# Kernel optimization log

Measured on AMD Instinct MI355X. Metric: run time of the kernel, lower is better.

The kernel has to match this reference:

```python
import jax, jax.numpy as jnp
import numpy as np

B, H_IMG, W_IMG = 8, 64, 64
C, HEADS, SR, MSG = 128, 4, 4, 4
N0 = H_IMG * W_IMG


def _linear(x, w, b):
    return x @ w.T + b


def _layernorm(x, g, b, eps=1e-5):
    mu = jnp.mean(x, -1, keepdims=True)
    var = jnp.mean(jnp.square(x - mu), -1, keepdims=True)
    return (x - mu) * jax.lax.rsqrt(var + eps) * g + b


def _conv2d(x, w, b, stride, pad, groups=1):
    y = jax.lax.conv_general_dilated(
        x, w, (stride, stride), [(pad, pad), (pad, pad)],
        dimension_numbers=("NCHW", "OIHW", "NCHW"), feature_group_count=groups)
    return y + b[None, :, None, None]


def setup_inputs():
    key = jax.random.key(0)
    ks = jax.random.split(key, 16)
    def nrm(k, shape, std=0.02):
        return jax.random.normal(k, shape, jnp.float32) * std
    z = lambda *s: jnp.zeros(s, jnp.float32)
    return {
        "x": jax.random.normal(ks[0], (B, N0, C), jnp.float32),
        "msg_tokens": jax.random.normal(ks[1], (B, MSG, C), jnp.float32),
        "Wq": nrm(ks[2], (C, C)), "bq": z(C),
        "sr1_w": nrm(ks[3], (C, C, 4, 4), float(np.sqrt(2.0 / (16 * C)))), "sr1_b": z(C),
        "ln1_g": jnp.ones((C,), jnp.float32), "ln1_b": z(C),
        "sr2_w": nrm(ks[4], (C, C, 2, 2), float(np.sqrt(2.0 / (4 * C)))), "sr2_b": z(C),
        "ln2_g": jnp.ones((C,), jnp.float32), "ln2_b": z(C),
        "kv1_w": nrm(ks[5], (C, C)), "kv1_b": z(C),
        "kv2_w": nrm(ks[6], (C, C)), "kv2_b": z(C),
        "lc1_w": nrm(ks[7], (C // 2, 1, 3, 3), float(np.sqrt(2.0 / 9.0))), "lc1_b": z(C // 2),
        "lc2_w": nrm(ks[8], (C // 2, 1, 3, 3), float(np.sqrt(2.0 / 9.0))), "lc2_b": z(C // 2),
        "proj_w": nrm(ks[9], (C, C)), "proj_b": z(C),
        "H": H_IMG, "W": W_IMG,
    }


def reference(x, msg_tokens, Wq, bq, sr1_w, sr1_b, ln1_g, ln1_b,
              sr2_w, sr2_b, ln2_g, ln2_b, kv1_w, kv1_b, kv2_w, kv2_b,
              lc1_w, lc1_b, lc2_w, lc2_b, proj_w, proj_b, H, W):
    Bsz, _, Cc = x.shape
    m = msg_tokens.shape[1]
    h = HEADS
    dh = Cc // h
    scale = dh ** -0.5
    x_q = jnp.concatenate([x, msg_tokens], axis=1)       # [B, N, C]
    N = x_q.shape[1]
    q = _linear(x_q, Wq, bq).reshape(Bsz, N, h, dh).transpose(0, 2, 1, 3)  # [B,h,N,dh]
    x_img = x.transpose(0, 2, 1).reshape(Bsz, Cc, H, W)

    def branch(sr_w, sr_b, ln_g, ln_b, kv_w, kv_b, lc_w, lc_b, q_half, stride):
        Hr, Wr = H // stride, W // stride
        L = Hr * Wr
        # spatial reduction conv -> tokens
        xr = _conv2d(x_img, sr_w, sr_b, stride, 0).reshape(Bsz, Cc, L).transpose(0, 2, 1)
        # message tokens pass through the SR conv via summed weights
        msg_r = jnp.einsum('bnc,oc->bno', msg_tokens, sr_w.sum((-1, -2))) + sr_b
        xk = jax.nn.gelu(_layernorm(jnp.concatenate([xr, msg_r], 1), ln_g, ln_b), approximate=False)
        kv = _linear(xk, kv_w, kv_b).reshape(Bsz, L + m, 2, h // 2, dh).transpose(2, 0, 3, 1, 4)
        k, v = kv[0], kv[1]                               # [B, h/2, L+m, dh]
        attn = jax.nn.softmax(jnp.einsum('bhnd,bhld->bhnl', q_half, k) * scale, axis=-1)
        # fused depthwise conv on the spatial part of V (message tokens bypass)
        v_flat = v.transpose(0, 2, 1, 3).reshape(Bsz, L + m, Cc // 2).transpose(0, 2, 1)  # [B,C/2,L+m]
        lc = _conv2d(v_flat[:, :, :L].reshape(Bsz, Cc // 2, Hr, Wr), lc_w, lc_b, 1, 1,
                     groups=Cc // 2).reshape(Bsz, Cc // 2, L)
        v_add = jnp.concatenate([lc, v_flat[:, :, L:]], axis=2)
        v = v + v_add.reshape(Bsz, h // 2, dh, L + m).transpose(0, 1, 3, 2)
        return jnp.einsum('bhnl,bhld->bhnd', attn, v).transpose(0, 2, 1, 3).reshape(Bsz, N, Cc // 2)

    x1 = branch(sr1_w, sr1_b, ln1_g, ln1_b, kv1_w, kv1_b, lc1_w, lc1_b, q[:, :h // 2], SR)
    x2 = branch(sr2_w, sr2_b, ln2_g, ln2_b, kv2_w, kv2_b, lc2_w, lc2_b, q[:, h // 2:], SR // 2)
    out = _linear(jnp.concatenate([x1, x2], -1), proj_w, proj_b)
    out = x_q + out                                       # identity = x_q, drop_path = Identity
    return out[:, :-m], out[:, -m:]
```

## Files before the change

kernel.cpp:

```cpp
#include <hip/hip_runtime.h>
#include <math.h>

#define BB 8
#define CC 128
#define N0 4096
#define MSGN 4
#define NTOT 4100
#define IMG 64
#define NPAD 4112
#define QTILES 257
#define LMP1 320
#define LMP2 1088

#define OFF_WFQ    0
#define OFF_WFKV1  8192
#define OFF_WFKV2  16384
#define OFF_WFPROJ 24576
#define OFF_WFSR1  32768
#define OFF_WFSR2  163840
#define OFF_QH     196608
#define OFF_XA     2301952
#define OFF_XK1    6565888
#define OFF_XK2    6701056
#define OFF_KV1O   7229440
#define OFF_KV2O   7495680
#define OFF_KH1    8548352
#define OFF_VT1    8630272
#define OFF_KH2    8712192
#define OFF_VT2    8990720

typedef _Float16 half8v __attribute__((ext_vector_type(8)));
typedef _Float16 half4v __attribute__((ext_vector_type(4)));
typedef float f32x4 __attribute__((ext_vector_type(4)));

__device__ __forceinline__ size_t af_idx(int m, int k, int Kc) {
    return ((size_t)((m >> 4) * Kc + (k >> 5)) * 64 + ((k >> 3) & 3) * 16 + (m & 15)) * 8 + (k & 7);
}

__global__ void prep_weights(const float* __restrict__ Wq, const float* __restrict__ kv1,
                             const float* __restrict__ kv2, const float* __restrict__ proj,
                             const float* __restrict__ sr1w, const float* __restrict__ sr2w,
                             float* __restrict__ ws, _Float16* __restrict__ Qh) {
    int u = blockIdx.x * blockDim.x + threadIdx.x;
    if (u >= 49152) {
        int idx = u - 49152;
        if (idx >= BB * 4 * (NPAD - NTOT) * 32) return;
        int d = idx & 31;
        int rest = idx >> 5;
        int n = NTOT + rest % (NPAD - NTOT);
        int rest2 = rest / (NPAD - NTOT);
        int hg = rest2 & 3;
        int b = rest2 >> 2;
        Qh[((size_t)(b * 4 + hg) * NPAD + n) * 32 + d] = (_Float16)0.f;
        return;
    }
    int seg, base;
    const float* w = nullptr;
    _Float16* dst;
    if (u < 2048)        { seg = 0; base = u;          w = Wq;   dst = (_Float16*)(ws + OFF_WFQ); }
    else if (u < 4096)   { seg = 0; base = u - 2048;   w = kv1;  dst = (_Float16*)(ws + OFF_WFKV1); }
    else if (u < 6144)   { seg = 0; base = u - 4096;   w = kv2;  dst = (_Float16*)(ws + OFF_WFKV2); }
    else if (u < 8192)   { seg = 0; base = u - 6144;   w = proj; dst = (_Float16*)(ws + OFF_WFPROJ); }
    else if (u < 40960)  { seg = 1; base = u - 8192;   w = sr1w; dst = (_Float16*)(ws + OFF_WFSR1); }
    else                 { seg = 2; base = u - 40960;  w = sr2w; dst = (_Float16*)(ws + OFF_WFSR2); }
    int lane = base & 63;
    int t = (base >> 6) & 7;
    int kc = base >> 9;
    int n = t * 16 + (lane & 15);
    int k0 = kc * 32 + (lane >> 4) * 8;
    half8v val;
    #pragma unroll
    for (int j = 0; j < 8; ++j) {
        int k = k0 + j;
        float v;
        if (seg == 0) v = w[n * 128 + k];
        else if (seg == 1) v = w[(n * 128 + (k & 127)) * 16 + (k >> 7)];
        else v = w[(n * 128 + (k & 127)) * 4 + (k >> 7)];
        val[j] = (_Float16)v;
    }
    *(half8v*)(dst + (size_t)base * 8) = val;
}

__global__ __launch_bounds__(256) void qproj_gemm(
    const float* __restrict__ x, const float* __restrict__ msg,
    const _Float16* __restrict__ Wf, const float* __restrict__ bias,
    _Float16* __restrict__ Qh) {
    int lane = threadIdx.x & 63, wave = threadIdx.x >> 6;
    int mt = blockIdx.x * 4 + wave;
    int m15 = lane & 15, quadk = lane >> 4;
    int m = mt * 16 + m15;
    bool valid = m < BB * NTOT;
    const float* rowp = x;
    if (valid) {
        int b = m / NTOT, n = m - b * NTOT;
        rowp = (n < N0) ? (x + ((size_t)b * N0 + n) * 128)
                        : (msg + ((size_t)b * MSGN + (n - N0)) * 128);
    }
    const half8v* Bp = (const half8v*)Wf + lane;
    f32x4 acc[8];
    #pragma unroll
    for (int t = 0; t < 8; ++t) acc[t] = (f32x4){0.f, 0.f, 0.f, 0.f};
    #pragma unroll
    for (int kc = 0; kc < 4; ++kc) {
        half8v a;
        if (valid) {
            const float4* p4 = (const float4*)(rowp + (kc * 4 + quadk) * 8);
            float4 f0 = p4[0], f1 = p4[1];
            a[0] = (_Float16)f0.x; a[1] = (_Float16)f0.y; a[2] = (_Float16)f0.z; a[3] = (_Float16)f0.w;
            a[4] = (_Float16)f1.x; a[5] = (_Float16)f1.y; a[6] = (_Float16)f1.z; a[7] = (_Float16)f1.w;
        } else {
            #pragma unroll
            for (int j = 0; j < 8; ++j) a[j] = (_Float16)0.f;
        }
        #pragma unroll
        for (int t = 0; t < 8; ++t)
            acc[t] = __builtin_amdgcn_mfma_f32_16x16x32_f16(a, Bp[(size_t)(kc * 8 + t) * 64], acc[t], 0, 0, 0);
    }
    int quad = lane >> 4, n15 = lane & 15;
    const float qscale = 0.17677669529663687f;
    #pragma unroll
    for (int r = 0; r < 4; ++r) {
        int mm = mt * 16 + quad * 4 + r;
        if (mm >= BB * NTOT) continue;
        int b = mm / NTOT, tok = mm - b * NTOT;
        #pragma unroll
        for (int t = 0; t < 8; ++t) {
            int n = t * 16 + n15;
            Qh[((size_t)(b * 4 + (n >> 5)) * NPAD + tok) * 32 + (n & 31)] =
                (_Float16)((acc[t][r] + bias[n]) * qscale);
        }
    }
}

template<int S, int WR, int LL, int LM, int KW>
__device__ __forceinline__ void sr_partial(
    int mtile, int kcbase, int lane, const float* __restrict__ x,
    const float* __restrict__ msg, const _Float16* __restrict__ Wf, f32x4 acc[8]) {
    int m15 = lane & 15, quadk = lane >> 4;
    int m = mtile * 16 + m15;
    bool valid = m < BB * LM;
    const float* base = x;
    bool isimg = false;
    if (valid) {
        int b = m / LM, tok = m - b * LM;
        if (tok < LL) {
            int hr = tok / WR, wr = tok - hr * WR;
            base = x + ((size_t)b * N0 + hr * S * IMG + wr * S) * 128;
            isimg = true;
        } else {
            base = msg + ((size_t)b * MSGN + (tok - LL)) * 128;
        }
    }
    const half8v* Bp = (const half8v*)Wf + lane;
    for (int kk = 0; kk < KW; ++kk) {
        int kc = kcbase + kk;
        int k0 = (kc * 4 + quadk) * 8;
        int c = k0 & 127, ij = k0 >> 7;
        half8v a;
        if (valid) {
            int off;
            if (isimg) {
                int ki = ij / S, kj = ij - ki * S;
                off = (ki * IMG + kj) * 128 + c;
            } else off = c;
            const float4* p4 = (const float4*)(base + off);
            float4 f0 = p4[0], f1 = p4[1];
            a[0] = (_Float16)f0.x; a[1] = (_Float16)f0.y; a[2] = (_Float16)f0.z; a[3] = (_Float16)f0.w;
            a[4] = (_Float16)f1.x; a[5] = (_Float16)f1.y; a[6] = (_Float16)f1.z; a[7] = (_Float16)f1.w;
        } else {
            #pragma unroll
            for (int j = 0; j < 8; ++j) a[j] = (_Float16)0.f;
        }
        #pragma unroll
        for (int t = 0; t < 8; ++t)
            acc[t] = __builtin_amdgcn_mfma_f32_16x16x32_f16(a, Bp[(size_t)(kc * 8 + t) * 64], acc[t], 0, 0, 0);
    }
}

__global__ __launch_bounds__(256) void sr_gemm(
    const float* __restrict__ x, const float* __restrict__ msg,
    const _Float16* __restrict__ Wf1, const _Float16* __restrict__ Wf2,
    const float* __restrict__ b1, const float* __restrict__ g1, const float* __restrict__ be1,
    const float* __restrict__ b2, const float* __restrict__ g2, const float* __restrict__ be2,
    _Float16* __restrict__ XK1, _Float16* __restrict__ XK2) {
    __shared__ float red[4][2048];
    int tid = threadIdx.x;
    int lane = tid & 63, wave = tid >> 6;
    int bid = blockIdx.x;
    f32x4 acc[8];
    #pragma unroll
    for (int t = 0; t < 8; ++t) acc[t] = (f32x4){0.f, 0.f, 0.f, 0.f};
    const float* bias;
    const float* lng;
    const float* lnb;
    _Float16* outp;
    int mtile, Mv;
    if (bid < 132) {
        mtile = bid; Mv = 2080;
        sr_partial<4, 16, 256, 260, 16>(mtile, wave * 16, lane, x, msg, Wf1, acc);
        bias = b1; lng = g1; lnb = be1; outp = XK1;
    } else {
        mtile = bid - 132; Mv = 8224;
        sr_partial<2, 32, 1024, 1028, 4>(mtile, wave * 4, lane, x, msg, Wf2, acc);
        bias = b2; lng = g2; lnb = be2; outp = XK2;
    }
    int quad = lane >> 4, n15 = lane & 15;
    #pragma unroll
    for (int t = 0; t < 8; ++t)
        #pragma unroll
        for (int r = 0; r < 4; ++r)
            red[wave][(quad * 4 + r) * 128 + t * 16 + n15] = acc[t][r];
    __syncthreads();
    for (int e = tid; e < 2048; e += 256)
        red[0][e] = red[0][e] + red[1][e] + red[2][e] + red[3][e];
    __syncthreads();
    int r16 = tid >> 4, l16 = tid & 15;
    int m = mtile * 16 + r16;
    float v[8];
    float s = 0.f;
    #pragma unroll
    for (int j = 0; j < 8; ++j) { v[j] = red[0][r16 * 128 + j * 16 + l16] + bias[j * 16 + l16]; s += v[j]; }
    #pragma unroll
    for (int off = 1; off < 16; off <<= 1) s += __shfl_xor(s, off);
    float mu = s * (1.f / 128.f);
    float q = 0.f;
    #pragma unroll
    for (int j = 0; j < 8; ++j) { v[j] -= mu; q += v[j] * v[j]; }
    #pragma unroll
    for (int off = 1; off < 16; off <<= 1) q += __shfl_xor(q, off);
    float rs = rsqrtf(q * (1.f / 128.f) + 1e-5f);
    if (m < Mv) {
        #pragma unroll
        for (int j = 0; j < 8; ++j) {
            int n = j * 16 + l16;
            float y = v[j] * rs * lng[n] + lnb[n];
            y = 0.5f * y * (1.f + erff(y * 0.70710678118654752f));
            outp[af_idx(m, n, 4)] = (_Float16)y;
        }
    }
}

__global__ __launch_bounds__(256) void kv_gemm(
    const _Float16* __restrict__ XK1, const _Float16* __restrict__ XK2,
    const _Float16* __restrict__ Wf1, const _Float16* __restrict__ Wf2,
    const float* __restrict__ b1, const float* __restrict__ b2,
    float* __restrict__ o1, float* __restrict__ o2) {
    int lane = threadIdx.x & 63, wave = threadIdx.x >> 6;
    int t = blockIdx.x * 4 + wave;
    int lt;
    const half8v* Ap;
    const half8v* Bp;
    const float* bias;
    float* outp;
    if (t < 130) { lt = t;       Ap = (const half8v*)XK1 + (size_t)lt * 4 * 64 + lane; Bp = (const half8v*)Wf1 + lane; bias = b1; outp = o1; }
    else         { lt = t - 130; Ap = (const half8v*)XK2 + (size_t)lt * 4 * 64 + lane; Bp = (const half8v*)Wf2 + lane; bias = b2; outp = o2; }
    f32x4 acc[8];
    #pragma unroll
    for (int tt = 0; tt < 8; ++tt) acc[tt] = (f32x4){0.f, 0.f, 0.f, 0.f};
    #pragma unroll
    for (int kc = 0; kc < 4; ++kc) {
        half8v a = Ap[(size_t)kc * 64];
        #pragma unroll
        for (int tt = 0; tt < 8; ++tt)
            acc[tt] = __builtin_amdgcn_mfma_f32_16x16x32_f16(a, Bp[(size_t)(kc * 8 + tt) * 64], acc[tt], 0, 0, 0);
    }
    int quad = lane >> 4, n15 = lane & 15;
    #pragma unroll
    for (int r = 0; r < 4; ++r) {
        int m = lt * 16 + quad * 4 + r;
        #pragma unroll
        for (int tt = 0; tt < 8; ++tt)
            outp[(size_t)m * 128 + tt * 16 + n15] = acc[tt][r] + bias[tt * 16 + n15];
    }
}

__global__ void pack_kv(const float* __restrict__ kv1o, const float* __restrict__ kv2o,
                        const float* __restrict__ lc1w, const float* __restrict__ lc1b,
                        const float* __restrict__ lc2w, const float* __restrict__ lc2b,
                        _Float16* __restrict__ Kh1, _Float16* __restrict__ Vt1,
                        _Float16* __restrict__ Kh2, _Float16* __restrict__ Vt2) {
    int idx = blockIdx.x * 256 + threadIdx.x;
    const int T1 = BB * LMP1 * 64;
    const float* kv;
    const float* lcw;
    const float* lcb;
    _Float16* Kh;
    _Float16* Vt;
    int Wr, L, Lm, Lmp, li;
    if (idx < T1) { li = idx;      kv = kv1o; lcw = lc1w; lcb = lc1b; Kh = Kh1; Vt = Vt1; Wr = 16; L = 256;  Lm = 260;  Lmp = LMP1; }
    else          { li = idx - T1; kv = kv2o; lcw = lc2w; lcb = lc2b; Kh = Kh2; Vt = Vt2; Wr = 32; L = 1024; Lm = 1028; Lmp = LMP2; }
    int ch = li & 63;
    int rest = li >> 6;
    int n = rest % Lmp;
    int b = rest / Lmp;
    int h2 = ch >> 5, d = ch & 31;
    int Hr = L / Wr;
    float kval = 0.f, vnew = 0.f;
    if (n < Lm) {
        const float* kvb = kv + (size_t)b * Lm * 128;
        kval = kvb[(size_t)n * 128 + ch];
        float v = kvb[(size_t)n * 128 + 64 + ch];
        float add;
        if (n < L) {
            int hr = n / Wr, wr = n - hr * Wr;
            float sum = lcb[ch];
            #pragma unroll
            for (int ki = 0; ki < 3; ++ki)
                #pragma unroll
                for (int kj = 0; kj < 3; ++kj) {
                    int y = hr + ki - 1, xx = wr + kj - 1;
                    if ((unsigned)y < (unsigned)Hr && (unsigned)xx < (unsigned)Wr)
                        sum += lcw[ch * 9 + ki * 3 + kj] * kvb[((size_t)y * Wr + xx) * 128 + 64 + ch];
                }
            add = sum;
        } else {
            add = v;
        }
        vnew = v + add;
    }
    Kh[((size_t)(b * 2 + h2) * Lmp + n) * 32 + d] = (_Float16)kval;
    Vt[(size_t)(b * 2 + h2) * Lmp * 32 + (size_t)(n >> 2) * 128 + d * 4 + (n & 3)] = (_Float16)vnew;
}

__global__ __launch_bounds__(256) void attn_mfma(
    const _Float16* __restrict__ Qh,
    const _Float16* __restrict__ Kh1, const _Float16* __restrict__ Vt1,
    const _Float16* __restrict__ Kh2, const _Float16* __restrict__ Vt2,
    _Float16* __restrict__ xcat) {
    int tid = threadIdx.x;
    int lane = tid & 63, wave = tid >> 6;
    int b = blockIdx.y;
    int h2 = blockIdx.z;
    int tile = blockIdx.x * 4 + wave;
    if (tile >= QTILES) return;
    int n0 = tile * 16;
    int q16 = lane & 15, quad = lane >> 4;
    const f32x4 zf = {0.f, 0.f, 0.f, 0.f};

    for (int br = 0; br < 2; ++br) {
        int Lmp = br ? LMP2 : LMP1;
        const _Float16* kb = (br ? Kh2 : Kh1) + (size_t)(b * 2 + h2) * Lmp * 32;
        const _Float16* vb = (br ? Vt2 : Vt1) + (size_t)(b * 2 + h2) * Lmp * 32;
        int hg = br * 2 + h2;
        half8v qf = *(const half8v*)(Qh + ((size_t)(b * 4 + hg) * NPAD + n0 + q16) * 32 + quad * 8);
        f32x4 O0 = {0.f, 0.f, 0.f, 0.f}, O1 = {0.f, 0.f, 0.f, 0.f};
        float l_part = 0.f;

        for (int k0 = 0; k0 < Lmp; k0 += 64) {
            f32x4 s4[4];
            #pragma unroll
            for (int i = 0; i < 4; ++i) {
                half8v kf = *(const half8v*)(kb + (size_t)(k0 + i * 16 + q16) * 32 + quad * 8);
                s4[i] = __builtin_amdgcn_mfma_f32_16x16x32_f16(kf, qf, zf, 0, 0, 0);
            }
            half4v pf[4];
            float ps = 0.f;
            #pragma unroll
            for (int i = 0; i < 4; ++i)
                #pragma unroll
                for (int r = 0; r < 4; ++r) {
                    float p = __expf(s4[i][r]);
                    ps += p;
                    pf[i][r] = (_Float16)p;
                }
            l_part += ps;
            #pragma unroll
            for (int i = 0; i < 4; ++i) {
                const _Float16* vbase = vb + (size_t)(((k0 + i * 16) >> 2) + quad) * 128 + q16 * 4;
                half4v v0 = *(const half4v*)(vbase);
                half4v v1 = *(const half4v*)(vbase + 64);
                O0 = __builtin_amdgcn_mfma_f32_16x16x16f16(pf[i], v0, O0, 0, 0, 0);
                O1 = __builtin_amdgcn_mfma_f32_16x16x16f16(pf[i], v1, O1, 0, 0, 0);
            }
        }

        float l = l_part;
        l += __shfl_xor(l, 16);
        l += __shfl_xor(l, 32);
        l -= 60.0f;
        float invl = 1.f / l;
        int kbase = br * 64 + h2 * 32;
        #pragma unroll
        for (int r = 0; r < 4; ++r) {
            float ir = __shfl(invl, quad * 4 + r);
            int n = n0 + quad * 4 + r;
            if (n < NTOT) {
                int m = b * NTOT + n;
                xcat[af_idx(m, kbase + q16, 4)] = (_Float16)(O0[r] * ir);
                xcat[af_idx(m, kbase + 16 + q16, 4)] = (_Float16)(O1[r] * ir);
            }
        }
    }
}

__global__ __launch_bounds__(256) void proj_gemm(
    const _Float16* __restrict__ Af, const _Float16* __restrict__ Wf,
    const float* __restrict__ bias, float* __restrict__ out_f32,
    const float* __restrict__ x, const float* __restrict__ msg) {
    int lane = threadIdx.x & 63, wave = threadIdx.x >> 6;
    int mt = blockIdx.x * 4 + wave;
    const half8v* Ap = (const half8v*)Af + (size_t)mt * 4 * 64 + lane;
    const half8v* Bp = (const half8v*)Wf + lane;
    f32x4 acc[8];
    #pragma unroll
    for (int t = 0; t < 8; ++t) acc[t] = (f32x4){0.f, 0.f, 0.f, 0.f};
    #pragma unroll
    for (int kc = 0; kc < 4; ++kc) {
        half8v a = Ap[(size_t)kc * 64];
        #pragma unroll
        for (int t = 0; t < 8; ++t)
            acc[t] = __builtin_amdgcn_mfma_f32_16x16x32_f16(a, Bp[(size_t)(kc * 8 + t) * 64], acc[t], 0, 0, 0);
    }
    int quad = lane >> 4, n15 = lane & 15;
    #pragma unroll
    for (int r = 0; r < 4; ++r) {
        int m = mt * 16 + quad * 4 + r;
        if (m >= BB * NTOT) continue;
        int b = m / NTOT, tok = m - b * NTOT;
        const float* rp;
        float* dst;
        if (tok < N0) {
            rp = x + ((size_t)b * N0 + tok) * 128;
            dst = out_f32 + ((size_t)b * N0 + tok) * 128;
        } else {
            rp = msg + ((size_t)b * MSGN + (tok - N0)) * 128;
            dst = out_f32 + (size_t)BB * N0 * 128 + ((size_t)b * MSGN + (tok - N0)) * 128;
        }
        #pragma unroll
        for (int t = 0; t < 8; ++t) {
            int n = t * 16 + n15;
            dst[n] = acc[t][r] + bias[n] + rp[n];
        }
    }
}

extern "C" void kernel_launch(void* const* d_in, const int* in_sizes, int n_in,
                              void* d_out, int out_size, void* d_ws, size_t ws_size,
                              hipStream_t stream) {
    const float* x     = (const float*)d_in[0];
    const float* msg   = (const float*)d_in[1];
    const float* Wq    = (const float*)d_in[2];
    const float* bq    = (const float*)d_in[3];
    const float* sr1w  = (const float*)d_in[4];
    const float* sr1b  = (const float*)d_in[5];
    const float* ln1g  = (const float*)d_in[6];
    const float* ln1b  = (const float*)d_in[7];
    const float* sr2w  = (const float*)d_in[8];
    const float* sr2b  = (const float*)d_in[9];
    const float* ln2g  = (const float*)d_in[10];
    const float* ln2b  = (const float*)d_in[11];
    const float* kv1w  = (const float*)d_in[12];
    const float* kv1b  = (const float*)d_in[13];
    const float* kv2w  = (const float*)d_in[14];
    const float* kv2b  = (const float*)d_in[15];
    const float* lc1w  = (const float*)d_in[16];
    const float* lc1b  = (const float*)d_in[17];
    const float* lc2w  = (const float*)d_in[18];
    const float* lc2b  = (const float*)d_in[19];
    const float* projw = (const float*)d_in[20];
    const float* projb = (const float*)d_in[21];
    float* ws  = (float*)d_ws;
    float* out = (float*)d_out;

    _Float16* WfQ    = (_Float16*)(ws + OFF_WFQ);
    _Float16* WfKV1  = (_Float16*)(ws + OFF_WFKV1);
    _Float16* WfKV2  = (_Float16*)(ws + OFF_WFKV2);
    _Float16* WfPROJ = (_Float16*)(ws + OFF_WFPROJ);
    _Float16* WfSR1  = (_Float16*)(ws + OFF_WFSR1);
    _Float16* WfSR2  = (_Float16*)(ws + OFF_WFSR2);
    _Float16* Qh     = (_Float16*)(ws + OFF_QH);
    _Float16* XA     = (_Float16*)(ws + OFF_XA);
    _Float16* XK1    = (_Float16*)(ws + OFF_XK1);
    _Float16* XK2    = (_Float16*)(ws + OFF_XK2);
    float* kv1o      = ws + OFF_KV1O;
    float* kv2o      = ws + OFF_KV2O;
    _Float16* Kh1    = (_Float16*)(ws + OFF_KH1);
    _Float16* Vt1    = (_Float16*)(ws + OFF_VT1);
    _Float16* Kh2    = (_Float16*)(ws + OFF_KH2);
    _Float16* Vt2    = (_Float16*)(ws + OFF_VT2);

    prep_weights<<<240, 256, 0, stream>>>(Wq, kv1w, kv2w, projw, sr1w, sr2w, ws, Qh);
    qproj_gemm<<<513, 256, 0, stream>>>(x, msg, WfQ, bq, Qh);
    sr_gemm<<<646, 256, 0, stream>>>(x, msg, WfSR1, WfSR2,
                                     sr1b, ln1g, ln1b, sr2b, ln2g, ln2b, XK1, XK2);
    kv_gemm<<<161, 256, 0, stream>>>(XK1, XK2, WfKV1, WfKV2, kv1b, kv2b, kv1o, kv2o);
    pack_kv<<<2816, 256, 0, stream>>>(kv1o, kv2o, lc1w, lc1b, lc2w, lc2b,
                                      Kh1, Vt1, Kh2, Vt2);
    attn_mfma<<<dim3(65, 8, 2), 256, 0, stream>>>(Qh, Kh1, Vt1, Kh2, Vt2, XA);
    proj_gemm<<<513, 256, 0, stream>>>(XA, WfPROJ, projb, out, x, msg);
}
```

Baseline: 216.0 us.

## Split attention over key range and merge partials in proj GEMM; fuse qproj into SR GEMM

Attention now runs with twice the blocks: each block processes half of the key/value range per branch and writes unnormalised partial outputs plus softmax denominators. The projection GEMM sums the two partials and divides by the combined denominator before its MFMA. The Q projection is also merged into the SR GEMM launch as extra blocks. The aim is better occupancy in attention and one fewer launch, at the cost of an extra partial-output buffer and more reads in proj_gemm. It also relies on a fixed max-free softmax offset and on the denominators of the two halves being directly summable.

```diff
diff --git a/kernel.cpp b/kernel.cpp
--- a/kernel.cpp
+++ b/kernel.cpp
@@ -19,15 +19,18 @@
 #define OFF_WFSR1  32768
 #define OFF_WFSR2  163840
 #define OFF_QH     196608
-#define OFF_XA     2301952
-#define OFF_XK1    6565888
-#define OFF_XK2    6701056
-#define OFF_KV1O   7229440
-#define OFF_KV2O   7495680
-#define OFF_KH1    8548352
-#define OFF_VT1    8630272
-#define OFF_KH2    8712192
-#define OFF_VT2    8990720
+#define OFF_XK1    2301952
+#define OFF_XK2    2435072
+#define OFF_KV1O   2961408
+#define OFF_KV2O   3227648
+#define OFF_KH1    4280320
+#define OFF_VT1    4362240
+#define OFF_KH2    4444160
+#define OFF_VT2    4722688
+#define OFF_XP0    5001216
+#define OFF_XP1    7102464
+#define OFF_L0     2301952
+#define OFF_L1     2433280
 
 typedef _Float16 half8v __attribute__((ext_vector_type(8)));
 typedef _Float16 half4v __attribute__((ext_vector_type(4)));
@@ -79,57 +82,6 @@
         val[j] = (_Float16)v;
     }
     *(half8v*)(dst + (size_t)base * 8) = val;
-}
-
-__global__ __launch_bounds__(256) void qproj_gemm(
-    const float* __restrict__ x, const float* __restrict__ msg,
-    const _Float16* __restrict__ Wf, const float* __restrict__ bias,
-    _Float16* __restrict__ Qh) {
-    int lane = threadIdx.x & 63, wave = threadIdx.x >> 6;
-    int mt = blockIdx.x * 4 + wave;
-    int m15 = lane & 15, quadk = lane >> 4;
-    int m = mt * 16 + m15;
-    bool valid = m < BB * NTOT;
-    const float* rowp = x;
-    if (valid) {
-        int b = m / NTOT, n = m - b * NTOT;
-        rowp = (n < N0) ? (x + ((size_t)b * N0 + n) * 128)
-                        : (msg + ((size_t)b * MSGN + (n - N0)) * 128);
-    }
-    const half8v* Bp = (const half8v*)Wf + lane;
-    f32x4 acc[8];
-    #pragma unroll
-    for (int t = 0; t < 8; ++t) acc[t] = (f32x4){0.f, 0.f, 0.f, 0.f};
-    #pragma unroll
-    for (int kc = 0; kc < 4; ++kc) {
-        half8v a;
-        if (valid) {
-            const float4* p4 = (const float4*)(rowp + (kc * 4 + quadk) * 8);
-            float4 f0 = p4[0], f1 = p4[1];
-            a[0] = (_Float16)f0.x; a[1] = (_Float16)f0.y; a[2] = (_Float16)f0.z; a[3] = (_Float16)f0.w;
-            a[4] = (_Float16)f1.x; a[5] = (_Float16)f1.y; a[6] = (_Float16)f1.z; a[7] = (_Float16)f1.w;
-        } else {
-            #pragma unroll
-            for (int j = 0; j < 8; ++j) a[j] = (_Float16)0.f;
-        }
-        #pragma unroll
-        for (int t = 0; t < 8; ++t)
-            acc[t] = __builtin_amdgcn_mfma_f32_16x16x32_f16(a, Bp[(size_t)(kc * 8 + t) * 64], acc[t], 0, 0, 0);
-    }
-    int quad = lane >> 4, n15 = lane & 15;
-    const float qscale = 0.17677669529663687f;
-    #pragma unroll
-    for (int r = 0; r < 4; ++r) {
-        int mm = mt * 16 + quad * 4 + r;
-        if (mm >= BB * NTOT) continue;
-        int b = mm / NTOT, tok = mm - b * NTOT;
-        #pragma unroll
-        for (int t = 0; t < 8; ++t) {
-            int n = t * 16 + n15;
-            Qh[((size_t)(b * 4 + (n >> 5)) * NPAD + tok) * 32 + (n & 31)] =
-                (_Float16)((acc[t][r] + bias[n]) * qscale);
-        }
-    }
 }
 
 template<int S, int WR, int LL, int LM, int KW>
@@ -177,16 +129,67 @@
     }
 }
 
-__global__ __launch_bounds__(256) void sr_gemm(
+__global__ __launch_bounds__(256) void input_gemms(
     const float* __restrict__ x, const float* __restrict__ msg,
     const _Float16* __restrict__ Wf1, const _Float16* __restrict__ Wf2,
     const float* __restrict__ b1, const float* __restrict__ g1, const float* __restrict__ be1,
     const float* __restrict__ b2, const float* __restrict__ g2, const float* __restrict__ be2,
-    _Float16* __restrict__ XK1, _Float16* __restrict__ XK2) {
+    _Float16* __restrict__ XK1, _Float16* __restrict__ XK2,
+    const _Float16* __restrict__ WfQ, const float* __restrict__ bq,
+    _Float16* __restrict__ Qh) {
     __shared__ float red[4][2048];
     int tid = threadIdx.x;
     int lane = tid & 63, wave = tid >> 6;
     int bid = blockIdx.x;
+
+    if (bid >= 646) {
+        int mt = (bid - 646) * 4 + wave;
+        int m15 = lane & 15, quadk = lane >> 4;
+        int m = mt * 16 + m15;
+        bool valid = m < BB * NTOT;
+        const float* rowp = x;
+        if (valid) {
+            int b = m / NTOT, n = m - b * NTOT;
+            rowp = (n < N0) ? (x + ((size_t)b * N0 + n) * 128)
+                            : (msg + ((size_t)b * MSGN + (n - N0)) * 128);
+        }
+        const half8v* Bp = (const half8v*)WfQ + lane;
+        f32x4 acc[8];
+        #pragma unroll
+        for (int t = 0; t < 8; ++t) acc[t] = (f32x4){0.f, 0.f, 0.f, 0.f};
+        #pragma unroll
+        for (int kc = 0; kc < 4; ++kc) {
+            half8v a;
+            if (valid) {
+                const float4* p4 = (const float4*)(rowp + (kc * 4 + quadk) * 8);
+                float4 f0 = p4[0], f1 = p4[1];
+                a[0] = (_Float16)f0.x; a[1] = (_Float16)f0.y; a[2] = (_Float16)f0.z; a[3] = (_Float16)f0.w;
+                a[4] = (_Float16)f1.x; a[5] = (_Float16)f1.y; a[6] = (_Float16)f1.z; a[7] = (_Float16)f1.w;
+            } else {
+                #pragma unroll
+                for (int j = 0; j < 8; ++j) a[j] = (_Float16)0.f;
+            }
+            #pragma unroll
+            for (int t = 0; t < 8; ++t)
+                acc[t] = __builtin_amdgcn_mfma_f32_16x16x32_f16(a, Bp[(size_t)(kc * 8 + t) * 64], acc[t], 0, 0, 0);
+        }
+        int quad = lane >> 4, n15 = lane & 15;
+        const float qscale = 0.17677669529663687f;
+        #pragma unroll
+        for (int r = 0; r < 4; ++r) {
+            int mm = mt * 16 + quad * 4 + r;
+            if (mm >= BB * NTOT) continue;
+            int b = mm / NTOT, tok = mm - b * NTOT;
+            #pragma unroll
+            for (int t = 0; t < 8; ++t) {
+                int n = t * 16 + n15;
+                Qh[((size_t)(b * 4 + (n >> 5)) * NPAD + tok) * 32 + (n & 31)] =
+                    (_Float16)((acc[t][r] + bq[n]) * qscale);
+            }
+        }
+        return;
+    }
+
     f32x4 acc[8];
     #pragma unroll
     for (int t = 0; t < 8; ++t) acc[t] = (f32x4){0.f, 0.f, 0.f, 0.f};
@@ -326,19 +329,25 @@
     const _Float16* __restrict__ Qh,
     const _Float16* __restrict__ Kh1, const _Float16* __restrict__ Vt1,
     const _Float16* __restrict__ Kh2, const _Float16* __restrict__ Vt2,
-    _Float16* __restrict__ xcat) {
+    _Float16* __restrict__ XP0, _Float16* __restrict__ XP1,
+    float* __restrict__ L0, float* __restrict__ L1) {
     int tid = threadIdx.x;
     int lane = tid & 63, wave = tid >> 6;
     int b = blockIdx.y;
-    int h2 = blockIdx.z;
+    int z = blockIdx.z;
+    int h2 = z & 1, h = z >> 1;
     int tile = blockIdx.x * 4 + wave;
     if (tile >= QTILES) return;
     int n0 = tile * 16;
     int q16 = lane & 15, quad = lane >> 4;
     const f32x4 zf = {0.f, 0.f, 0.f, 0.f};
+    _Float16* xp = h ? XP1 : XP0;
+    float* Lp = h ? L1 : L0;
 
     for (int br = 0; br < 2; ++br) {
         int Lmp = br ? LMP2 : LMP1;
+        int k_lo = h ? (br ? 576 : 192) : 0;
+        int k_hi = br ? (h ? 1088 : 576) : (h ? 320 : 192);
         const _Float16* kb = (br ? Kh2 : Kh1) + (size_t)(b * 2 + h2) * Lmp * 32;
         const _Float16* vb = (br ? Vt2 : Vt1) + (size_t)(b * 2 + h2) * Lmp * 32;
         int hg = br * 2 + h2;
@@ -346,7 +355,7 @@
         f32x4 O0 = {0.f, 0.f, 0.f, 0.f}, O1 = {0.f, 0.f, 0.f, 0.f};
         float l_part = 0.f;
 
-        for (int k0 = 0; k0 < Lmp; k0 += 64) {
+        for (int k0 = k_lo; k0 < k_hi; k0 += 64) {
             f32x4 s4[4];
             #pragma unroll
             for (int i = 0; i < 4; ++i) {
@@ -377,36 +386,54 @@
         float l = l_part;
         l += __shfl_xor(l, 16);
         l += __shfl_xor(l, 32);
-        l -= 60.0f;
-        float invl = 1.f / l;
+        if (h) l -= 60.0f;
+        if (quad == 0) {
+            int n = n0 + q16;
+            if (n < NTOT) Lp[(size_t)(b * NTOT + n) * 4 + hg] = l;
+        }
         int kbase = br * 64 + h2 * 32;
         #pragma unroll
         for (int r = 0; r < 4; ++r) {
-            float ir = __shfl(invl, quad * 4 + r);
             int n = n0 + quad * 4 + r;
             if (n < NTOT) {
                 int m = b * NTOT + n;
-                xcat[af_idx(m, kbase + q16, 4)] = (_Float16)(O0[r] * ir);
-                xcat[af_idx(m, kbase + 16 + q16, 4)] = (_Float16)(O1[r] * ir);
+                xp[af_idx(m, kbase + q16, 4)] = (_Float16)O0[r];
+                xp[af_idx(m, kbase + 16 + q16, 4)] = (_Float16)O1[r];
             }
         }
     }
 }
 
 __global__ __launch_bounds__(256) void proj_gemm(
-    const _Float16* __restrict__ Af, const _Float16* __restrict__ Wf,
-    const float* __restrict__ bias, float* __restrict__ out_f32,
-    const float* __restrict__ x, const float* __restrict__ msg) {
+    const _Float16* __restrict__ XP0, const _Float16* __restrict__ XP1,
+    const float* __restrict__ L0, const float* __restrict__ L1,
+    const _Float16* __restrict__ Wf, const float* __restrict__ bias,
+    float* __restrict__ out_f32, const float* __restrict__ x, const float* __restrict__ msg) {
     int lane = threadIdx.x & 63, wave = threadIdx.x >> 6;
     int mt = blockIdx.x * 4 + wave;
-    const half8v* Ap = (const half8v*)Af + (size_t)mt * 4 * 64 + lane;
+    const half8v* Ap0 = (const half8v*)XP0 + (size_t)mt * 4 * 64 + lane;
+    const half8v* Ap1 = (const half8v*)XP1 + (size_t)mt * 4 * 64 + lane;
     const half8v* Bp = (const half8v*)Wf + lane;
+    int m15 = lane & 15;
+    int mrow = mt * 16 + m15;
+    bool lvalid = mrow < BB * NTOT;
     f32x4 acc[8];
     #pragma unroll
     for (int t = 0; t < 8; ++t) acc[t] = (f32x4){0.f, 0.f, 0.f, 0.f};
     #pragma unroll
     for (int kc = 0; kc < 4; ++kc) {
-        half8v a = Ap[(size_t)kc * 64];
+        half8v a0 = Ap0[(size_t)kc * 64];
+        half8v a1 = Ap1[(size_t)kc * 64];
+        float inv = 0.f;
+        if (lvalid) {
+            float l0 = L0[(size_t)mrow * 4 + kc];
+            float l1 = L1[(size_t)mrow * 4 + kc];
+            inv = 1.f / (l0 + l1);
+        }
+        half8v a;
+        #pragma unroll
+        for (int j = 0; j < 8; ++j)
+            a[j] = (_Float16)(((float)a0[j] + (float)a1[j]) * inv);
         #pragma unroll
         for (int t = 0; t < 8; ++t)
             acc[t] = __builtin_amdgcn_mfma_f32_16x16x32_f16(a, Bp[(size_t)(kc * 8 + t) * 64], acc[t], 0, 0, 0);
@@ -469,7 +496,10 @@
     _Float16* WfSR1  = (_Float16*)(ws + OFF_WFSR1);
     _Float16* WfSR2  = (_Float16*)(ws + OFF_WFSR2);
     _Float16* Qh     = (_Float16*)(ws + OFF_QH);
-    _Float16* XA     = (_Float16*)(ws + OFF_XA);
+    _Float16* XP0    = (_Float16*)(ws + OFF_XP0);
+    _Float16* XP1    = (_Float16*)(ws + OFF_XP1);
+    float* L0        = ws + OFF_L0;
+    float* L1        = ws + OFF_L1;
     _Float16* XK1    = (_Float16*)(ws + OFF_XK1);
     _Float16* XK2    = (_Float16*)(ws + OFF_XK2);
     float* kv1o      = ws + OFF_KV1O;
@@ -480,12 +510,13 @@
     _Float16* Vt2    = (_Float16*)(ws + OFF_VT2);
 
     prep_weights<<<240, 256, 0, stream>>>(Wq, kv1w, kv2w, projw, sr1w, sr2w, ws, Qh);
-    qproj_gemm<<<513, 256, 0, stream>>>(x, msg, WfQ, bq, Qh);
-    sr_gemm<<<646, 256, 0, stream>>>(x, msg, WfSR1, WfSR2,
-                                     sr1b, ln1g, ln1b, sr2b, ln2g, ln2b, XK1, XK2);
+    input_gemms<<<1159, 256, 0, stream>>>(x, msg, WfSR1, WfSR2,
+                                          sr1b, ln1g, ln1b, sr2b, ln2g, ln2b,
+                                          XK1, XK2, WfQ, bq, Qh);
     kv_gemm<<<161, 256, 0, stream>>>(XK1, XK2, WfKV1, WfKV2, kv1b, kv2b, kv1o, kv2o);
     pack_kv<<<2816, 256, 0, stream>>>(kv1o, kv2o, lc1w, lc1b, lc2w, lc2b,
                                       Kh1, Vt1, Kh2, Vt2);
-    attn_mfma<<<dim3(65, 8, 2), 256, 0, stream>>>(Qh, Kh1, Vt1, Kh2, Vt2, XA);
-    proj_gemm<<<513, 256, 0, stream>>>(XA, WfPROJ, projb, out, x, msg);
-}
+    attn_mfma<<<dim3(65, 8, 4), 256, 0, stream>>>(Qh, Kh1, Vt1, Kh2, Vt2,
+                                                  XP0, XP1, L0, L1);
+    proj_gemm<<<513, 256, 0, stream>>>(XP0, XP1, L0, L1, WfPROJ, projb, out, x, msg);
+}
```

After: 212.6 us. No clear change (-1.6%).
